# Performance work log

Measured on AMD Instinct MI355X. Metric: run time of the kernel, lower is better.

## Reference

```python
import jax, jax.numpy as jnp
import numpy as np

B, N, E = 64, 2048, 32768
F_IN, NHID, RULES = 256, 512, 128
RATIO = 0.5
K1 = int(np.ceil(RATIO * N)); K2 = int(np.ceil(RATIO * K1)); K3 = int(np.ceil(RATIO * K2))


def _gcn(x, src, dst, em, W, b):
    # GCNConv with self-loops and symmetric normalization; em is a float edge-validity mask.
    n = x.shape[0]
    h = x @ W  # [n, out]
    deg = jax.ops.segment_sum(em, dst, num_segments=n) + 1.0  # in-degree + self-loop
    dinv = jax.lax.rsqrt(deg)
    coef = dinv[src] * dinv[dst] * em  # [E]
    agg = jax.ops.segment_sum(h[src] * coef[:, None], dst, num_segments=n)
    return agg + h / deg[:, None] + b  # second term = self-loop with norm 1/deg


def _sag_pool(x, src, dst, em, Wg, bg, k):
    # SAGPooling: GCN scorer, per-graph top-k, scale kept nodes by tanh(score), filter+reindex edges.
    n = x.shape[0]
    score = _gcn(x, src, dst, em, Wg, bg)[:, 0]  # [n]
    vals, perm = jax.lax.top_k(score, k)
    xk = x[perm] * jnp.tanh(vals)[:, None]  # [k, F]
    newidx = jnp.full((n,), -1, dtype=src.dtype).at[perm].set(jnp.arange(k, dtype=src.dtype))
    ns, nd = newidx[src], newidx[dst]
    keep = em * (ns >= 0).astype(em.dtype) * (nd >= 0).astype(em.dtype)
    return xk, jnp.maximum(ns, 0), jnp.maximum(nd, 0), keep


_gcn_b = jax.vmap(_gcn, in_axes=(0, 0, 0, 0, None, None))
_pool_b = jax.vmap(_sag_pool, in_axes=(0, 0, 0, 0, None, None, None))


def setup_inputs() -> dict:
    key = jax.random.key(0)
    ks = jax.random.split(key, 16)
    def w(k, shape, fan_in):
        return jax.random.normal(k, shape, jnp.float32) * (1.0 / np.sqrt(fan_in))
    return {
        "x": jax.random.normal(ks[0], (B, N, F_IN), jnp.float32),
        "src": jax.random.randint(ks[1], (B, E), 0, N, jnp.int32),
        "dst": jax.random.randint(ks[2], (B, E), 0, N, jnp.int32),
        "W1": w(ks[3], (F_IN, NHID), F_IN), "b1": jnp.zeros((NHID,), jnp.float32),
        "Wp1": w(ks[4], (NHID, 1), NHID), "bp1": jnp.zeros((1,), jnp.float32),
        "W2": w(ks[5], (NHID, NHID), NHID), "b2": jnp.zeros((NHID,), jnp.float32),
        "Wp2": w(ks[6], (NHID, 1), NHID), "bp2": jnp.zeros((1,), jnp.float32),
        "W3": w(ks[7], (NHID, NHID), NHID), "b3": jnp.zeros((NHID,), jnp.float32),
        "Wp3": w(ks[8], (NHID, 1), NHID), "bp3": jnp.zeros((1,), jnp.float32),
        "lin1_W": w(ks[9], (2 * NHID, NHID), 2 * NHID), "lin1_b": jnp.zeros((NHID,), jnp.float32),
        "lin2_W": w(ks[10], (NHID, NHID // 2), NHID), "lin2_b": jnp.zeros((NHID // 2,), jnp.float32),
        "pi_W": w(ks[11], (NHID // 2, RULES), NHID // 2), "pi_b": jnp.zeros((RULES,), jnp.float32),
        "v_W": w(ks[12], (NHID // 2, 1), NHID // 2), "v_b": jnp.zeros((1,), jnp.float32),
    }


def reference(x, src, dst, W1, b1, Wp1, bp1, W2, b2, Wp2, bp2, W3, b3, Wp3, bp3,
              lin1_W, lin1_b, lin2_W, lin2_b, pi_W, pi_b, v_W, v_b):
    em = jnp.ones(src.shape, x.dtype)
    h = jax.nn.relu(_gcn_b(x, src, dst, em, W1, b1))
    h, s, d, em = _pool_b(h, src, dst, em, Wp1, bp1, K1)
    x1 = jnp.concatenate([h.max(axis=1), h.mean(axis=1)], axis=1)  # [B, 2*NHID]
    h = jax.nn.relu(_gcn_b(h, s, d, em, W2, b2))
    h, s, d, em = _pool_b(h, s, d, em, Wp2, bp2, K2)
    x2 = jnp.concatenate([h.max(axis=1), h.mean(axis=1)], axis=1)
    h = jax.nn.relu(_gcn_b(h, s, d, em, W3, b3))
    h, s, d, em = _pool_b(h, s, d, em, Wp3, bp3, K3)
    x3 = jnp.concatenate([h.max(axis=1), h.mean(axis=1)], axis=1)
    z = x1 + x2 + x3
    z = jax.nn.relu(z @ lin1_W + lin1_b)
    z = jax.nn.relu(z @ lin2_W + lin2_b)
    pi = jax.nn.log_softmax(z @ pi_W + pi_b, axis=1)
    v = jax.nn.relu(z @ v_W + v_b)
    return pi, v
```

## Files before the change

kernel.cpp:

```cpp
#include <hip/hip_runtime.h>
#include <math.h>
#include <cstdint>

#define B_   64
#define N_   2048
#define E_   32768
#define FIN  256
#define H_   512

typedef __bf16 bf16x8 __attribute__((ext_vector_type(8)));
typedef float  f32x4  __attribute__((ext_vector_type(4)));

__device__ __forceinline__ unsigned short f2bf(float f) {
  unsigned u = __float_as_uint(f);
  u += 0x7FFF + ((u >> 16) & 1);
  return (unsigned short)(u >> 16);
}
__device__ __forceinline__ unsigned pk2(float a, float b) {
  return (unsigned)f2bf(a) | ((unsigned)f2bf(b) << 16);
}
__device__ __forceinline__ float bflo(unsigned u) { return __uint_as_float(u << 16); }
__device__ __forceinline__ float bfhi(unsigned u) { return __uint_as_float(u & 0xFFFF0000u); }

__device__ __forceinline__ void accum8(float* acc, uint4 u, float c) {
  acc[0] += c * bflo(u.x); acc[1] += c * bfhi(u.x);
  acc[2] += c * bflo(u.y); acc[3] += c * bfhi(u.y);
  acc[4] += c * bflo(u.z); acc[5] += c * bfhi(u.z);
  acc[6] += c * bflo(u.w); acc[7] += c * bfhi(u.w);
}

__device__ __forceinline__ void glds16(const void* g, void* l) {
  __builtin_amdgcn_global_load_lds(
      (const __attribute__((address_space(1))) unsigned int*)g,
      (__attribute__((address_space(3))) unsigned int*)l, 16, 0, 0);
}

__global__ void xcvt_k(const float* __restrict__ x, unsigned short* __restrict__ xb) {
  int i = blockIdx.x * 256 + threadIdx.x;
  float4 f = reinterpret_cast<const float4*>(x)[i];
  uint2 o; o.x = pk2(f.x, f.y); o.y = pk2(f.z, f.w);
  reinterpret_cast<uint2*>(xb)[i] = o;
}

__global__ void wcvt_k(const float* __restrict__ W, unsigned short* __restrict__ Wt, int K) {
  int idx = blockIdx.x * 256 + threadIdx.x;
  int k = idx >> 9, n = idx & 511;
  Wt[n * K + k] = f2bf(W[idx]);
}

__global__ __launch_bounds__(256) void gemm_mfma(
    const unsigned short* __restrict__ Xb,
    const int* __restrict__ perm, const float* __restrict__ tanhv,
    const unsigned short* __restrict__ Wt, unsigned short* __restrict__ Y,
    int K, int kl2, int nsl2,
    const float* __restrict__ bias, const float* __restrict__ wp, float* __restrict__ hs) {
  __shared__ uint4 As[512];
  __shared__ uint4 Bs[512];
  const int tid = threadIdx.x;
  const int w = tid >> 6, L = tid & 63;
  const int bid = blockIdx.x;
  const int xcd = bid & 7;
  const int t = bid >> 3;
  const int colb = t & 3;
  const int strip = ((t >> 2) << 3) + xcd;
  const int m0 = strip * 128;
  const int n0 = colb * 128;
  const int e = L & 15, q = L >> 4;

  const int sw3 = (L >> 3) & 7;
  const int cA = (w * 64 + L) ^ sw3;
  const int rloc = cA >> 2;
  const int kcs = (cA & 3) * 8;

  f32x4 acc[4][4];
#pragma unroll
  for (int j = 0; j < 4; j++)
#pragma unroll
    for (int nn = 0; nn < 4; nn++) acc[j][nn] = (f32x4){0.f, 0.f, 0.f, 0.f};

  size_t asrc[2];
#pragma unroll
  for (int i = 0; i < 2; i++) {
    int g = m0 + i * 64 + rloc;
    size_t row;
    if (perm) {
      int b = g >> kl2;
      int node = perm[g];
      row = (size_t)(b << nsl2) + node;
    } else {
      row = (size_t)g;
    }
    asrc[i] = row * (size_t)K + kcs;
  }
  size_t bsrc[2];
#pragma unroll
  for (int i = 0; i < 2; i++) bsrc[i] = (size_t)(n0 + i * 64 + rloc) * K + kcs;

  const int fo = e * 4 + q;
  const int fosw = fo ^ (fo >> 3);

  for (int k0 = 0; k0 < K; k0 += 32) {
    glds16(Xb + asrc[0] + k0, &As[0 * 256 + w * 64]);
    glds16(Xb + asrc[1] + k0, &As[1 * 256 + w * 64]);
    glds16(Wt + bsrc[0] + k0, &Bs[0 * 256 + w * 64]);
    glds16(Wt + bsrc[1] + k0, &Bs[1 * 256 + w * 64]);
    __syncthreads();
    bf16x8 af[4], bfr[4];
#pragma unroll
    for (int j = 0; j < 4; j++) af[j]  = __builtin_bit_cast(bf16x8, As[((w & 1) * 4 + j) * 64 + fosw]);
#pragma unroll
    for (int j = 0; j < 4; j++) bfr[j] = __builtin_bit_cast(bf16x8, Bs[((w >> 1) * 4 + j) * 64 + fosw]);
#pragma unroll
    for (int j = 0; j < 4; j++)
#pragma unroll
      for (int nn = 0; nn < 4; nn++)
        acc[j][nn] = __builtin_amdgcn_mfma_f32_16x16x32_bf16(af[j], bfr[nn], acc[j][nn], 0, 0, 0);
    __syncthreads();
  }
  float bs[4], wsv[4];
#pragma unroll
  for (int nn = 0; nn < 4; nn++) {
    int coly = n0 + ((w >> 1) * 4 + nn) * 16 + e;
    bs[nn]  = bias ? bias[coly] : 0.f;
    wsv[nn] = wp ? wp[coly] : 0.f;
  }
#pragma unroll
  for (int j = 0; j < 4; j++) {
    int mt = (w & 1) * 4 + j;
#pragma unroll
    for (int r = 0; r < 4; r++) {
      int grow = m0 + mt * 16 + q * 4 + r;
      float t2 = tanhv ? tanhv[grow] : 1.0f;
      float p = 0.f;
#pragma unroll
      for (int nn = 0; nn < 4; nn++) {
        int coly = n0 + ((w >> 1) * 4 + nn) * 16 + e;
        float v = acc[j][nn][r] * t2;
        if (bias) v = fmaxf(v + bs[nn], 0.f);
        Y[(size_t)grow * 512 + coly] = f2bf(v);
        p += v * wsv[nn];
      }
      if (wp) {
        p += __shfl_xor(p, 1, 64); p += __shfl_xor(p, 2, 64);
        p += __shfl_xor(p, 4, 64); p += __shfl_xor(p, 8, 64);
        if ((L & 15) == 0) atomicAdd(&hs[grow], p);
      }
    }
  }
}

__global__ void count_k(const int* __restrict__ dst, int* __restrict__ cnt, int nl2) {
  int g = blockIdx.x * 256 + threadIdx.x;
  int d = dst[g];
  if (d < 0) return;
  int b = g >> 15;
  atomicAdd(&cnt[(b << nl2) + d], 1);
}

__global__ __launch_bounds__(256) void scan_k(const int* __restrict__ cnt,
                                              int* __restrict__ rowptr, int* __restrict__ cursor,
                                              float* __restrict__ deg, float* __restrict__ dinv, int n) {
  int b = blockIdx.x, tid = threadIdx.x;
  __shared__ int ls[2048];
  __shared__ int ch[256];
  int per = n >> 8;
  int base = tid * per;
  int s = 0;
  for (int i = 0; i < per; i++) { int v = cnt[b * n + base + i]; ls[base + i] = v; s += v; }
  ch[tid] = s;
  __syncthreads();
  for (int off = 1; off < 256; off <<= 1) {
    int v = (tid >= off) ? ch[tid - off] : 0;
    __syncthreads();
    ch[tid] += v;
    __syncthreads();
  }
  int run = (tid == 0) ? 0 : ch[tid - 1];
  for (int i = 0; i < per; i++) {
    int v = ls[base + i];
    rowptr[b * (n + 1) + base + i] = run;
    cursor[b * n + base + i] = run;
    float d = (float)(v + 1);
    deg[b * n + base + i] = d;
    dinv[b * n + base + i] = 1.0f / sqrtf(d);
    run += v;
  }
  if (tid == 255) rowptr[b * (n + 1) + n] = run;
}

__global__ void fill_k(const int* __restrict__ src, const int* __restrict__ dst,
                       const float* __restrict__ dinv, int* cursor, int* col,
                       float* ce, int nl2) {
  int g = blockIdx.x * 256 + threadIdx.x;
  int d = dst[g];
  if (d < 0) return;
  int b = g >> 15;
  int s = src[g];
  int pos = atomicAdd(&cursor[(b << nl2) + d], 1);
  col[(b << 15) + pos] = s;
  ce[(b << 15) + pos] = dinv[(b << nl2) + s] * dinv[(b << nl2) + d];
}

__global__ __launch_bounds__(256) void aggx_k(
    const unsigned short* __restrict__ X,
    const int* __restrict__ rowptr, const int* __restrict__ col,
    const float* __restrict__ ce, const float* __restrict__ deg,
    unsigned short* __restrict__ Xa) {
  const int w = threadIdx.x >> 6, L = threadIdx.x & 63;
  const int xcd = blockIdx.x & 7;
  const int slot = blockIdx.x >> 3;
  const int gslot = slot >> 9;
  const int v4 = slot & 511;
  const int b = (gslot << 3) + xcd;
  const int v = v4 * 4 + w;
  const int bbase = b << 11;
  const int vg = bbase + v;
  const int rb = b * (N_ + 1) + v;
  const int st = rowptr[rb], en = rowptr[rb + 1];
  const int* cb = col + (b << 15);
  const float* cee = ce + (b << 15);
  const int h = L >> 5, hl = L & 31;
  const unsigned short* Xb_ = X + (size_t)bbase * 256 + hl * 8;
  const int T = en - st + 1;
  const float selfc = 1.0f / deg[vg];
  float acc[8] = {0.f, 0.f, 0.f, 0.f, 0.f, 0.f, 0.f, 0.f};
  for (int t = h; t < T; t += 2) {
    bool isE = (t < T - 1);
    int s = isE ? cb[st + t] : v;
    float c = isE ? cee[st + t] : selfc;
    uint4 u = *(const uint4*)(Xb_ + (size_t)s * 256);
    accum8(acc, u, c);
  }
#pragma unroll
  for (int i = 0; i < 8; i++) acc[i] += __shfl_xor(acc[i], 32, 64);
  if (h == 0) {
    uint4 o;
    o.x = pk2(acc[0], acc[1]); o.y = pk2(acc[2], acc[3]);
    o.z = pk2(acc[4], acc[5]); o.w = pk2(acc[6], acc[7]);
    *(uint4*)(Xa + (size_t)vg * 256 + hl * 8) = o;
  }
}

template <int NL2>
__global__ __launch_bounds__(256) void agg_k(
    const unsigned short* __restrict__ H,
    const int* __restrict__ rowptr, const int* __restrict__ col,
    const float* __restrict__ ce, const float* __restrict__ deg,
    const float* __restrict__ bias, const float* __restrict__ wp,
    unsigned short* __restrict__ C, float* __restrict__ hs) {
  const int n = 1 << NL2;
  const int xcd = blockIdx.x & 7;
  const int slot = blockIdx.x >> 3;
  const int gslot = slot >> (NL2 - 2);
  const int v4 = slot & ((1 << (NL2 - 2)) - 1);
  const int b = (gslot << 3) + xcd;
  const int w = threadIdx.x >> 6, L = threadIdx.x & 63;
  const int v = v4 * 4 + w;
  const int bbase = b << NL2;
  const int vg = bbase + v;
  const int rb = b * (n + 1) + v;
  const int st = rowptr[rb], en = rowptr[rb + 1];
  const int* cb = col + (b << 15);
  const float* cee = ce + (b << 15);
  const unsigned short* Hb_ = H + (size_t)bbase * 512 + (size_t)L * 8;

  float acc[8] = {0.f, 0.f, 0.f, 0.f, 0.f, 0.f, 0.f, 0.f};
  int e2 = st;
  for (; e2 + 4 <= en; e2 += 4) {
    int s0 = cb[e2], s1 = cb[e2 + 1], s2 = cb[e2 + 2], s3 = cb[e2 + 3];
    float c0 = cee[e2], c1 = cee[e2 + 1], c2 = cee[e2 + 2], c3 = cee[e2 + 3];
    uint4 u0 = *(const uint4*)(Hb_ + (size_t)s0 * 512);
    uint4 u1 = *(const uint4*)(Hb_ + (size_t)s1 * 512);
    uint4 u2 = *(const uint4*)(Hb_ + (size_t)s2 * 512);
    uint4 u3 = *(const uint4*)(Hb_ + (size_t)s3 * 512);
    accum8(acc, u0, c0); accum8(acc, u1, c1);
    accum8(acc, u2, c2); accum8(acc, u3, c3);
  }
  for (; e2 < en; e2++) {
    int s = cb[e2];
    uint4 u = *(const uint4*)(Hb_ + (size_t)s * 512);
    accum8(acc, u, cee[e2]);
  }
  {
    float idg = 1.0f / deg[vg];
    uint4 u = *(const uint4*)(Hb_ + (size_t)v * 512);
    accum8(acc, u, idg);
  }
  float4 bLo = *(const float4*)(bias + L * 8);
  float4 bHi = *(const float4*)(bias + L * 8 + 4);
  acc[0] = fmaxf(acc[0] + bLo.x, 0.f); acc[1] = fmaxf(acc[1] + bLo.y, 0.f);
  acc[2] = fmaxf(acc[2] + bLo.z, 0.f); acc[3] = fmaxf(acc[3] + bLo.w, 0.f);
  acc[4] = fmaxf(acc[4] + bHi.x, 0.f); acc[5] = fmaxf(acc[5] + bHi.y, 0.f);
  acc[6] = fmaxf(acc[6] + bHi.z, 0.f); acc[7] = fmaxf(acc[7] + bHi.w, 0.f);
  uint4 o;
  o.x = pk2(acc[0], acc[1]); o.y = pk2(acc[2], acc[3]);
  o.z = pk2(acc[4], acc[5]); o.w = pk2(acc[6], acc[7]);
  *(uint4*)(C + (size_t)vg * 512 + L * 8) = o;
  float4 wLo = *(const float4*)(wp + L * 8);
  float4 wHi = *(const float4*)(wp + L * 8 + 4);
  float p = acc[0] * wLo.x + acc[1] * wLo.y + acc[2] * wLo.z + acc[3] * wLo.w
          + acc[4] * wHi.x + acc[5] * wHi.y + acc[6] * wHi.z + acc[7] * wHi.w;
#pragma unroll
  for (int off = 32; off > 0; off >>= 1) p += __shfl_down(p, off, 64);
  if (L == 0) hs[vg] = p;
}

__global__ void scoreagg_k(const float* __restrict__ hs, const int* __restrict__ rowptr,
                           const int* __restrict__ col, const float* __restrict__ ce,
                           const float* __restrict__ deg, const float* __restrict__ bp,
                           float* __restrict__ score, int nl2) {
  int idx = blockIdx.x * 256 + threadIdx.x;
  int n = 1 << nl2;
  int b = idx >> nl2, v = idx & (n - 1);
  int rb = b * (n + 1) + v;
  int st = rowptr[rb], en = rowptr[rb + 1];
  const int* cb = col + (b << 15);
  const float* cee = ce + (b << 15);
  int bbase = b << nl2;
  float acc = 0.f;
  int e = st;
  for (; e + 4 <= en; e += 4) {
    acc += hs[bbase + cb[e]] * cee[e] + hs[bbase + cb[e + 1]] * cee[e + 1]
         + hs[bbase + cb[e + 2]] * cee[e + 2] + hs[bbase + cb[e + 3]] * cee[e + 3];
  }
  for (; e < en; e++) acc += hs[bbase + cb[e]] * cee[e];
  score[idx] = acc + hs[idx] / deg[idx] + bp[0];
}

__global__ __launch_bounds__(1024) void topk_k(const float* __restrict__ score, int* __restrict__ perm,
                                               float* __restrict__ tanhv, int* __restrict__ newidx,
                                               int n, int k) {
  int b = blockIdx.x, tid = threadIdx.x;
  __shared__ float ss[2048];
  __shared__ int si[2048];
  for (int i = tid; i < n; i += 1024) { ss[i] = score[b * n + i]; si[i] = i; }
  __syncthreads();
  for (int size = 2; size <= n; size <<= 1) {
    for (int stride = size >> 1; stride > 0; stride >>= 1) {
      for (int i = tid; i < n; i += 1024) {
        int j = i ^ stride;
        if (j > i) {
          bool up = ((i & size) == 0);
          float fi = ss[i], fj = ss[j];
          int ii = si[i], ij = si[j];
          bool iBefore = (fi > fj) || (fi == fj && ii < ij);
          bool sw = up ? (!iBefore) : iBefore;
          if (sw) { ss[i] = fj; ss[j] = fi; si[i] = ij; si[j] = ii; }
        }
      }
      __syncthreads();
    }
  }
  for (int r = tid; r < n; r += 1024) newidx[b * n + si[r]] = (r < k) ? r : -1;
  for (int r = tid; r < k; r += 1024) { perm[b * k + r] = si[r]; tanhv[b * k + r] = tanhf(ss[r]); }
}

__global__ void reindex_count_k(const int* srcO, const int* dstO, const int* newidx,
                                int* srcN, int* dstN, int* cnt, int nl2new) {
  int g = blockIdx.x * 256 + threadIdx.x;
  int b = g >> 15;
  int dd = dstO[g];
  int sN = 0, dN = -1;
  if (dd >= 0) {
    int ns = newidx[(b << (nl2new + 1)) + srcO[g]];
    int nd = newidx[(b << (nl2new + 1)) + dd];
    if (ns >= 0 && nd >= 0) {
      sN = ns; dN = nd;
      atomicAdd(&cnt[(b << nl2new) + nd], 1);
    }
  }
  srcN[g] = sN; dstN[g] = dN;
}

__global__ __launch_bounds__(512) void statsp_k(const unsigned short* __restrict__ C,
    const int* __restrict__ perm, const float* __restrict__ tv,
    float* __restrict__ zp, int nsl2, int k, int kch) {
  int b = blockIdx.x, rg = blockIdx.y, f = threadIdx.x;
  int r0 = rg * kch;
  float mx = -1e30f, sm = 0.f;
#pragma unroll 4
  for (int r = r0; r < r0 + kch; r++) {
    int node = perm[b * k + r];
    float t = tv[b * k + r];
    float val = __uint_as_float((unsigned)C[((size_t)((b << nsl2) + node)) * 512 + f] << 16) * t;
    mx = fmaxf(mx, val); sm += val;
  }
  zp[(size_t)(b * 8 + rg) * 1024 + f] = mx;
  zp[(size_t)(b * 8 + rg) * 1024 + 512 + f] = sm;
}

__global__ __launch_bounds__(512) void statsr_k(const float* __restrict__ zp,
                                                float* __restrict__ z, int k) {
  int b = blockIdx.x, f = threadIdx.x;
  float mx = -1e30f, sm = 0.f;
#pragma unroll
  for (int g = 0; g < 8; g++) {
    mx = fmaxf(mx, zp[(size_t)(b * 8 + g) * 1024 + f]);
    sm += zp[(size_t)(b * 8 + g) * 1024 + 512 + f];
  }
  z[b * 1024 + f] += mx;
  z[b * 1024 + 512 + f] += sm / (float)k;
}

__global__ __launch_bounds__(256) void mlp1_k(const float* __restrict__ z,
                                              const float* __restrict__ W1,
                                              float* __restrict__ zp1) {
  const int kc = blockIdx.x & 7;
  const int b = blockIdx.x >> 3;
  const int tid = threadIdx.x;
  __shared__ float zs[128];
  if (tid < 128) zs[tid] = z[b * 1024 + kc * 128 + tid];
  __syncthreads();
  float a0 = 0.f, a1 = 0.f;
  const float* Wb = W1 + (size_t)(kc * 128) * 512 + tid * 2;
#pragma unroll 4
  for (int i = 0; i < 128; i++) {
    float2 w = *(const float2*)(Wb + (size_t)i * 512);
    float zi = zs[i];
    a0 += zi * w.x; a1 += zi * w.y;
  }
  reinterpret_cast<float2*>(zp1 + ((size_t)(kc * 64 + b)) * 512)[tid] = make_float2(a0, a1);
}

__global__ __launch_bounds__(256) void mlp2_k(const float* __restrict__ zp1,
                                              const float* __restrict__ b1,
                                              const float* __restrict__ W2,
                                              float* __restrict__ zp2) {
  const int kc = blockIdx.x & 1;
  const int b = blockIdx.x >> 1;
  const int tid = threadIdx.x;
  __shared__ float z1s[256];
  {
    int i = kc * 256 + tid;
    float a = b1[i];
#pragma unroll
    for (int g = 0; g < 8; g++) a += zp1[((size_t)(g * 64 + b)) * 512 + i];
    z1s[tid] = fmaxf(a, 0.f);
  }
  __syncthreads();
  float a = 0.f;
  const float* Wb = W2 + (size_t)(kc * 256) * 256 + tid;
#pragma unroll 4
  for (int i = 0; i < 256; i++) a += z1s[i] * Wb[(size_t)i * 256];
  zp2[((size_t)(kc * 64 + b)) * 256 + tid] = a;
}

__global__ __launch_bounds__(128) void mlp3_k(const float* __restrict__ zp2,
                                              const float* __restrict__ b2,
                                              const float* __restrict__ piW,
                                              const float* __restrict__ pib,
                                              const float* __restrict__ vW,
                                              const float* __restrict__ vb,
                                              float* __restrict__ out) {
  const int b = blockIdx.x, tid = threadIdx.x;
  __shared__ float z2s[256];
  __shared__ float wred[4];
  __shared__ float sred[2];
  for (int t = tid; t < 256; t += 128) {
    float a = b2[t] + zp2[(size_t)b * 256 + t] + zp2[(size_t)(64 + b) * 256 + t];
    z2s[t] = fmaxf(a, 0.f);
  }
  __syncthreads();
  float a = pib[tid];
#pragma unroll 4
  for (int i = 0; i < 256; i++) a += z2s[i] * piW[(size_t)i * 128 + tid];
  float vp = z2s[tid] * vW[tid] + z2s[tid + 128] * vW[tid + 128];
  float m = a;
#pragma unroll
  for (int off = 32; off > 0; off >>= 1) {
    vp += __shfl_xor(vp, off, 64);
    m = fmaxf(m, __shfl_xor(m, off, 64));
  }
  const int wv = tid >> 6;
  if ((tid & 63) == 0) { wred[wv] = m; wred[2 + wv] = vp; }
  __syncthreads();
  m = fmaxf(wred[0], wred[1]);
  float s = expf(a - m);
#pragma unroll
  for (int off = 32; off > 0; off >>= 1) s += __shfl_xor(s, off, 64);
  if ((tid & 63) == 0) sred[wv] = s;
  __syncthreads();
  s = sred[0] + sred[1];
  if (tid == 0) out[B_ * 128 + b] = fmaxf(vb[0] + wred[2] + wred[3], 0.f);
  out[b * 128 + tid] = a - m - logf(s);
}

extern "C" void kernel_launch(void* const* d_in, const int* in_sizes, int n_in,
                              void* d_out, int out_size, void* d_ws, size_t ws_size,
                              hipStream_t stream) {
  const float* x    = (const float*)d_in[0];
  const int*   src0 = (const int*)d_in[1];
  const int*   dst0 = (const int*)d_in[2];
  const float* W1   = (const float*)d_in[3];
  const float* b1   = (const float*)d_in[4];
  const float* Wp1  = (const float*)d_in[5];
  const float* bp1  = (const float*)d_in[6];
  const float* W2   = (const float*)d_in[7];
  const float* b2   = (const float*)d_in[8];
  const float* Wp2  = (const float*)d_in[9];
  const float* bp2  = (const float*)d_in[10];
  const float* W3   = (const float*)d_in[11];
  const float* b3   = (const float*)d_in[12];
  const float* Wp3  = (const float*)d_in[13];
  const float* bp3  = (const float*)d_in[14];
  const float* l1W  = (const float*)d_in[15];
  const float* l1b  = (const float*)d_in[16];
  const float* l2W  = (const float*)d_in[17];
  const float* l2b  = (const float*)d_in[18];
  const float* piW  = (const float*)d_in[19];
  const float* pib  = (const float*)d_in[20];
  const float* vW   = (const float*)d_in[21];
  const float* vb   = (const float*)d_in[22];
  float* out = (float*)d_out;
  (void)in_sizes; (void)n_in; (void)out_size; (void)ws_size;

  unsigned short* Cb = (unsigned short*)d_in[0];

  char* base = (char*)d_ws;
  size_t off = 0;
  auto alloc = [&](size_t bytes) -> void* {
    void* r = base + off;
    off += (bytes + 255) & ~(size_t)255;
    return r;
  };
  unsigned short* Hb   = (unsigned short*)alloc((size_t)B_ * 1024 * H_ * 2);
  unsigned short* xb   = (unsigned short*)alloc((size_t)B_ * N_ * FIN * 2);
  unsigned short* Xa   = (unsigned short*)alloc((size_t)B_ * N_ * FIN * 2);
  unsigned short* W1t  = (unsigned short*)alloc((size_t)512 * 256 * 2);
  unsigned short* W2t  = (unsigned short*)alloc((size_t)512 * 512 * 2);
  unsigned short* W3t  = (unsigned short*)alloc((size_t)512 * 512 * 2);
  int*   srcA   = (int*)alloc((size_t)B_ * E_ * 4);
  int*   dstA   = (int*)alloc((size_t)B_ * E_ * 4);
  int*   col    = (int*)alloc((size_t)B_ * E_ * 4);
  float* coefE  = (float*)alloc((size_t)B_ * E_ * 4);
  int*   cnt    = (int*)alloc((size_t)B_ * N_ * 4);
  int*   cursor = (int*)alloc((size_t)B_ * N_ * 4);
  int*   rowptr = (int*)alloc((size_t)B_ * (N_ + 1) * 4);
  float* deg    = (float*)alloc((size_t)B_ * N_ * 4);
  float* dinv   = (float*)alloc((size_t)B_ * N_ * 4);
  float* hs     = (float*)alloc((size_t)B_ * N_ * 4);
  float* score  = (float*)alloc((size_t)B_ * N_ * 4);
  int*   newidx = (int*)alloc((size_t)B_ * N_ * 4);
  int*   perm   = (int*)alloc((size_t)B_ * 1024 * 4);
  float* tanhv  = (float*)alloc((size_t)B_ * 1024 * 4);
  float* zpart  = (float*)alloc((size_t)B_ * 8 * 1024 * 4);
  float* z      = (float*)alloc((size_t)B_ * 1024 * 4);

  float* zp1 = zpart;
  float* zp2 = zpart + (size_t)8 * 64 * 512;

  const int EB = B_ * E_ / 256;

  xcvt_k<<<B_ * N_ * FIN / 4 / 256, 256, 0, stream>>>(x, xb);
  wcvt_k<<<256 * 512 / 256, 256, 0, stream>>>(W1, W1t, 256);
  wcvt_k<<<512 * 512 / 256, 256, 0, stream>>>(W2, W2t, 512);
  wcvt_k<<<512 * 512 / 256, 256, 0, stream>>>(W3, W3t, 512);
  hipMemsetAsync(z, 0, (size_t)B_ * 1024 * 4, stream);

  {
    hipMemsetAsync(cnt, 0, (size_t)B_ * 2048 * 4, stream);
    count_k<<<EB, 256, 0, stream>>>(dst0, cnt, 11);
    scan_k<<<B_, 256, 0, stream>>>(cnt, rowptr, cursor, deg, dinv, 2048);
    fill_k<<<EB, 256, 0, stream>>>(src0, dst0, dinv, cursor, col, coefE, 11);
    aggx_k<<<B_ * 2048 / 4, 256, 0, stream>>>(xb, rowptr, col, coefE, deg, Xa);
    hipMemsetAsync(hs, 0, (size_t)B_ * 2048 * 4, stream);
    gemm_mfma<<<B_ * 2048 / 128 * 4, 256, 0, stream>>>(
        Xa, nullptr, nullptr, W1t, Cb, 256, 0, 0, b1, Wp1, hs);
    scoreagg_k<<<B_ * 2048 / 256, 256, 0, stream>>>(hs, rowptr, col, coefE, deg, bp1, score, 11);
    topk_k<<<B_, 1024, 0, stream>>>(score, perm, tanhv, newidx, 2048, 1024);
    statsp_k<<<dim3(B_, 8), 512, 0, stream>>>(Cb, perm, tanhv, zpart, 11, 1024, 128);
    statsr_k<<<B_, 512, 0, stream>>>(zpart, z, 1024);
    hipMemsetAsync(cnt, 0, (size_t)B_ * 1024 * 4, stream);
    reindex_count_k<<<EB, 256, 0, stream>>>(src0, dst0, newidx, srcA, dstA, cnt, 10);
    scan_k<<<B_, 256, 0, stream>>>(cnt, rowptr, cursor, deg, dinv, 1024);
    fill_k<<<EB, 256, 0, stream>>>(srcA, dstA, dinv, cursor, col, coefE, 10);
  }
  {
    gemm_mfma<<<B_ * 1024 / 128 * 4, 256, 0, stream>>>(
        Cb, perm, tanhv, W2t, Hb, 512, 10, 11, nullptr, nullptr, nullptr);
    agg_k<10><<<B_ * 1024 / 4, 256, 0, stream>>>(Hb, rowptr, col, coefE, deg, b2, Wp2, Cb, hs);
    scoreagg_k<<<B_ * 1024 / 256, 256, 0, stream>>>(hs, rowptr, col, coefE, deg, bp2, score, 10);
    topk_k<<<B_, 1024, 0, stream>>>(score, perm, tanhv, newidx, 1024, 512);
    statsp_k<<<dim3(B_, 8), 512, 0, stream>>>(Cb, perm, tanhv, zpart, 10, 512, 64);
    statsr_k<<<B_, 512, 0, stream>>>(zpart, z, 512);
    hipMemsetAsync(cnt, 0, (size_t)B_ * 512 * 4, stream);
    reindex_count_k<<<EB, 256, 0, stream>>>(srcA, dstA, newidx, srcA, dstA, cnt, 9);
    scan_k<<<B_, 256, 0, stream>>>(cnt, rowptr, cursor, deg, dinv, 512);
    fill_k<<<EB, 256, 0, stream>>>(srcA, dstA, dinv, cursor, col, coefE, 9);
  }
  {
    gemm_mfma<<<B_ * 512 / 128 * 4, 256, 0, stream>>>(
        Cb, perm, tanhv, W3t, Hb, 512, 9, 10, nullptr, nullptr, nullptr);
    agg_k<9><<<B_ * 512 / 4, 256, 0, stream>>>(Hb, rowptr, col, coefE, deg, b3, Wp3, Cb, hs);
    scoreagg_k<<<B_ * 512 / 256, 256, 0, stream>>>(hs, rowptr, col, coefE, deg, bp3, score, 9);
    topk_k<<<B_, 1024, 0, stream>>>(score, perm, tanhv, newidx, 512, 256);
    statsp_k<<<dim3(B_, 8), 512, 0, stream>>>(Cb, perm, tanhv, zpart, 9, 256, 32);
    statsr_k<<<B_, 512, 0, stream>>>(zpart, z, 256);
  }

  mlp1_k<<<B_ * 8, 256, 0, stream>>>(z, l1W, zp1);
  mlp2_k<<<B_ * 2, 256, 0, stream>>>(zp1, l1b, l2W, zp2);
  mlp3_k<<<B_, 128, 0, stream>>>(zp2, l2b, piW, pib, vW, vb, out);
}
```

Baseline: 1.070 ms.

## Double-buffer GEMM LDS tiles and stage epilogue through LDS for vector stores

The MFMA GEMM's LDS tiles are now double-buffered, so the next k-slice's global-to-LDS loads are issued while the current slice is being multiplied. This removes one barrier per iteration and hides load latency. The epilogue now writes bf16 results into a padded LDS tile and then copies them out with coalesced 16-byte row stores, replacing the scattered 2-byte global stores. The cost is more LDS per block (about 34 KB), which may reduce occupancy.

```diff
diff --git a/kernel.cpp b/kernel.cpp
--- a/kernel.cpp
+++ b/kernel.cpp
@@ -54,8 +54,7 @@
     const unsigned short* __restrict__ Wt, unsigned short* __restrict__ Y,
     int K, int kl2, int nsl2,
     const float* __restrict__ bias, const float* __restrict__ wp, float* __restrict__ hs) {
-  __shared__ uint4 As[512];
-  __shared__ uint4 Bs[512];
+  __shared__ __align__(16) char smem[34816];
   const int tid = threadIdx.x;
   const int w = tid >> 6, L = tid & 63;
   const int bid = blockIdx.x;
@@ -98,13 +97,31 @@
 
   const int fo = e * 4 + q;
   const int fosw = fo ^ (fo >> 3);
-
-  for (int k0 = 0; k0 < K; k0 += 32) {
-    glds16(Xb + asrc[0] + k0, &As[0 * 256 + w * 64]);
-    glds16(Xb + asrc[1] + k0, &As[1 * 256 + w * 64]);
-    glds16(Wt + bsrc[0] + k0, &Bs[0 * 256 + w * 64]);
-    glds16(Wt + bsrc[1] + k0, &Bs[1 * 256 + w * 64]);
-    __syncthreads();
+  const int lofs = w * 64 * 16;
+
+  const int nk = K >> 5;
+  {
+    char* Ab = smem;
+    char* Bb = smem + 16384;
+    glds16(Xb + asrc[0], Ab + 0 * 4096 + lofs);
+    glds16(Xb + asrc[1], Ab + 1 * 4096 + lofs);
+    glds16(Wt + bsrc[0], Bb + 0 * 4096 + lofs);
+    glds16(Wt + bsrc[1], Bb + 1 * 4096 + lofs);
+  }
+  __syncthreads();
+  int cur = 0;
+  for (int kt = 0; kt < nk; ++kt) {
+    if (kt + 1 < nk) {
+      const int k0 = (kt + 1) << 5;
+      char* Ab = smem + (cur ^ 1) * 8192;
+      char* Bb = smem + 16384 + (cur ^ 1) * 8192;
+      glds16(Xb + asrc[0] + k0, Ab + 0 * 4096 + lofs);
+      glds16(Xb + asrc[1] + k0, Ab + 1 * 4096 + lofs);
+      glds16(Wt + bsrc[0] + k0, Bb + 0 * 4096 + lofs);
+      glds16(Wt + bsrc[1] + k0, Bb + 1 * 4096 + lofs);
+    }
+    const uint4* As = (const uint4*)(smem + cur * 8192);
+    const uint4* Bs = (const uint4*)(smem + 16384 + cur * 8192);
     bf16x8 af[4], bfr[4];
 #pragma unroll
     for (int j = 0; j < 4; j++) af[j]  = __builtin_bit_cast(bf16x8, As[((w & 1) * 4 + j) * 64 + fosw]);
@@ -116,7 +133,11 @@
       for (int nn = 0; nn < 4; nn++)
         acc[j][nn] = __builtin_amdgcn_mfma_f32_16x16x32_bf16(af[j], bfr[nn], acc[j][nn], 0, 0, 0);
     __syncthreads();
-  }
+    cur ^= 1;
+  }
+
+  const int RS = 136;
+  unsigned short* Csm = (unsigned short*)smem;
   float bs[4], wsv[4];
 #pragma unroll
   for (int nn = 0; nn < 4; nn++) {
@@ -129,15 +150,16 @@
     int mt = (w & 1) * 4 + j;
 #pragma unroll
     for (int r = 0; r < 4; r++) {
-      int grow = m0 + mt * 16 + q * 4 + r;
+      int lrow = mt * 16 + q * 4 + r;
+      int grow = m0 + lrow;
       float t2 = tanhv ? tanhv[grow] : 1.0f;
       float p = 0.f;
 #pragma unroll
       for (int nn = 0; nn < 4; nn++) {
-        int coly = n0 + ((w >> 1) * 4 + nn) * 16 + e;
+        int lcol = (w >> 1) * 64 + nn * 16 + e;
         float v = acc[j][nn][r] * t2;
         if (bias) v = fmaxf(v + bs[nn], 0.f);
-        Y[(size_t)grow * 512 + coly] = f2bf(v);
+        Csm[lrow * RS + lcol] = f2bf(v);
         p += v * wsv[nn];
       }
       if (wp) {
@@ -146,6 +168,14 @@
         if ((L & 15) == 0) atomicAdd(&hs[grow], p);
       }
     }
+  }
+  __syncthreads();
+  const int rbase = tid >> 4, ci = tid & 15;
+#pragma unroll
+  for (int pass = 0; pass < 8; ++pass) {
+    int lrow = pass * 16 + rbase;
+    uint4 u = *(const uint4*)(Csm + lrow * RS + ci * 8);
+    *(uint4*)(Y + (size_t)(m0 + lrow) * 512 + n0 + ci * 8) = u;
   }
 }
 
```

Result: no change. 1.071 ms (+0.1%).
